# Optimization experiments

Measured on AMD Instinct MI355X. Metric: run time of the kernel, lower is better.

## Reference

```python
import jax, jax.numpy as jnp
import numpy as np

EOS = 130


def setup_inputs() -> dict:
    key = jax.random.key(0)
    ks = jax.random.split(key, 16)
    B, H, W, C = 32, 12, 32, 512   # encoder feature map
    V, E, D = 600, 256, 512        # vocab, embed_dim, decoder_hidden
    T = 192
    s = lambda *d: 1.0 / np.sqrt(d[-1])
    inp = {
        "encoder_outputs": jax.random.normal(ks[0], (B, H, W, C), jnp.float32),
        "tgt_tokens": jax.random.randint(ks[1], (B, T), 0, V, jnp.int64),
        # embedding table (padding_idx=0 row zeroed)
        "emb_table": (jax.random.normal(ks[2], (V, E), jnp.float32) * 0.02).at[0].set(0.0),
        # LSTMCell params, gate order i,f,g,o; stored (in, 4D) / (4D,)
        "W_ih": jax.random.normal(ks[3], (E + D, 4 * D), jnp.float32) * s(E + D),
        "b_ih": jnp.zeros((4 * D,), jnp.float32),
        "W_hh": jax.random.normal(ks[4], (D, 4 * D), jnp.float32) * s(D),
        "b_hh": jnp.zeros((4 * D,), jnp.float32),
        # attention
        "W_h": jax.random.normal(ks[5], (D, D), jnp.float32) * s(D),
        "W_v": jax.random.normal(ks[6], (C, D), jnp.float32) * s(C),
        "v": jax.random.normal(ks[7], (D, 1), jnp.float32) * s(D),
        # output path
        "W_c": jax.random.normal(ks[8], (D + C, D), jnp.float32) * s(D + C),
        "b_c": jnp.zeros((D,), jnp.float32),
        "W_out": jax.random.normal(ks[9], (D, V), jnp.float32) * s(D),
        "b_out": jnp.zeros((V,), jnp.float32),
    }
    return inp


def _decode(encoder_outputs, tgt_tokens, emb_table, W_ih, b_ih, W_hh, b_hh,
            W_h, W_v, v, W_c, b_c, W_out, b_out):
    B, H, W_, C = encoder_outputs.shape
    D = W_h.shape[0]
    enc = encoder_outputs.reshape(B, H * W_, C)          # (B, N, C)
    Wv = enc @ W_v                                       # (B, N, D) precompute (step-invariant)

    def step(carry, tok_t):
        hx, cx, o_prev, input_token, finished = carry
        emb = emb_table[input_token]                     # (B, E)
        rnn_in = jnp.concatenate([emb, o_prev], axis=-1)
        gates = rnn_in @ W_ih + b_ih + hx @ W_hh + b_hh  # (B, 4D)
        i, f, g, o = jnp.split(gates, 4, axis=-1)
        cx = jax.nn.sigmoid(f) * cx + jax.nn.sigmoid(i) * jnp.tanh(g)
        hx = jax.nn.sigmoid(o) * jnp.tanh(cx)
        # Bahdanau attention
        score = jnp.squeeze(jnp.tanh(hx[:, None, :] @ W_h + Wv) @ v, -1)  # (B, N)
        alpha = jax.nn.softmax(score, axis=1)
        context = jnp.einsum('bn,bnc->bc', alpha, enc)
        o_t = jnp.tanh(jnp.concatenate([hx, context], axis=-1) @ W_c + b_c)
        logits_t = o_t @ W_out + b_out                   # (B, V)
        next_token = tok_t                               # teacher forcing (ratio=1.0)
        finished = finished | (next_token == EOS)
        input_token = jnp.where(finished, 0, next_token)
        return (hx, cx, o_t, input_token, finished), (logits_t, alpha)

    hx = jnp.zeros((B, D), encoder_outputs.dtype)
    cx = jnp.zeros_like(hx)
    o0 = jnp.zeros_like(hx)
    tok0 = jnp.zeros((B,), tgt_tokens.dtype)             # sos_index = 0
    fin0 = jnp.zeros((B,), bool)
    xs = tgt_tokens[:, 1:].T                             # (T-1, B)
    _, (logits, alphas) = jax.lax.scan(step, (hx, cx, o0, tok0, fin0), xs)
    return logits.transpose(1, 0, 2), alphas.transpose(1, 0, 2)  # (B,T-1,V), (B,T-1,N)


def reference(encoder_outputs, tgt_tokens, emb_table, W_ih, b_ih, W_hh, b_hh,
              W_h, W_v, v, W_c, b_c, W_out, b_out):
    return _decode(encoder_outputs, tgt_tokens, emb_table, W_ih, b_ih, W_hh, b_hh,
                   W_h, W_v, v, W_c, b_c, W_out, b_out)
```

## Files before the change

kernel.cpp:

```cpp
#include <hip/hip_runtime.h>
#include <cstdint>

#define Bb 32
#define Cc 512
#define Nn 384
#define Vv 600
#define Ee 256
#define Dd 512
#define Tt 192
#define Ss 191
#define EOS_TOK 130
#define BD (Bb*Dd)
#define NBLK 256
#define NTHR 512

#define OFF_TOK   0
#define OFF_SHIFT 8192
#define OFF_WV    8256
#define OFF_HXT   6299712
#define OFF_XO    6332480
#define OFF_HXB   6348864
#define OFF_DEN   6365248
#define OFF_Q     6373440
#define OFF_CTXB  6389824
#define OFF_OBUF  6406208
#define OFF_BAR   9551936

#define LOGITS_SZ (Bb*Ss*Vv)
#define ALPHA_SZ  (Bb*Ss*Nn)

__device__ __forceinline__ float sigm_(float x) {
    float e = __expf(-x);
    return __builtin_amdgcn_rcpf(1.0f + e);
}
__device__ __forceinline__ float tanh_(float x) {
    float xc = fminf(15.0f, fmaxf(-15.0f, x));
    float e = __expf(2.0f * xc);
    return (e - 1.0f) * __builtin_amdgcn_rcpf(e + 1.0f);
}

__device__ __forceinline__ void st_dev(float* p, float v) {
    __hip_atomic_store(p, v, __ATOMIC_RELAXED, __HIP_MEMORY_SCOPE_AGENT);
}
__device__ __forceinline__ float ld1_dev(const float* p) {
    return __hip_atomic_load(p, __ATOMIC_RELAXED, __HIP_MEMORY_SCOPE_AGENT);
}
__device__ __forceinline__ float2 ld2_dev(const float* p) {
    unsigned long long u = __hip_atomic_load((const unsigned long long*)p,
                                             __ATOMIC_RELAXED,
                                             __HIP_MEMORY_SCOPE_AGENT);
    float2 f;
    f.x = __uint_as_float((unsigned int)u);
    f.y = __uint_as_float((unsigned int)(u >> 32));
    return f;
}

__device__ __forceinline__ void gbar(int* flags, int* genv, int ibar) {
    __syncthreads();
    const int target = ibar + 1;
    if (threadIdx.x == 0)
        __hip_atomic_store(&flags[blockIdx.x * 16], target, __ATOMIC_RELAXED,
                           __HIP_MEMORY_SCOPE_AGENT);
    if (blockIdx.x == 0) {
        if (threadIdx.x < 64) {
            int l = threadIdx.x * 4;
            for (;;) {
                int f0 = __hip_atomic_load(&flags[(l + 0) * 16], __ATOMIC_RELAXED,
                                           __HIP_MEMORY_SCOPE_AGENT);
                int f1 = __hip_atomic_load(&flags[(l + 1) * 16], __ATOMIC_RELAXED,
                                           __HIP_MEMORY_SCOPE_AGENT);
                int f2 = __hip_atomic_load(&flags[(l + 2) * 16], __ATOMIC_RELAXED,
                                           __HIP_MEMORY_SCOPE_AGENT);
                int f3 = __hip_atomic_load(&flags[(l + 3) * 16], __ATOMIC_RELAXED,
                                           __HIP_MEMORY_SCOPE_AGENT);
                if (__all(f0 >= target && f1 >= target &&
                          f2 >= target && f3 >= target)) break;
                __builtin_amdgcn_s_sleep(1);
            }
            if (threadIdx.x < 32)
                __hip_atomic_store(&genv[threadIdx.x * 16], target,
                                   __ATOMIC_RELAXED, __HIP_MEMORY_SCOPE_AGENT);
        }
    } else if (threadIdx.x == 0) {
        int* g = &genv[(blockIdx.x >> 3) * 16];
        while (__hip_atomic_load(g, __ATOMIC_RELAXED,
                                 __HIP_MEMORY_SCOPE_AGENT) < target)
            __builtin_amdgcn_s_sleep(2);
    }
    __syncthreads();
}

__device__ __forceinline__ void poll8(int* base, int grp, int target) {
    if (threadIdx.x < 64) {
        int* g = &base[(grp * 8 + (threadIdx.x & 7)) * 16];
        while (__hip_atomic_load(g, __ATOMIC_RELAXED,
                                 __HIP_MEMORY_SCOPE_AGENT) < target)
            __builtin_amdgcn_s_sleep(1);
    }
    __syncthreads();
}

__global__ void k_setup(const int* __restrict__ tgt, const float* __restrict__ vv,
                        float* zbase, int* bar, int* tok, float* shiftbuf) {
    int gid = blockIdx.x * 256 + threadIdx.x;
    for (int i = gid; i < 73728; i += 96 * 256) zbase[i] = 0.f;
    if (gid < 12800) bar[gid] = 0;
    if (blockIdx.x == 0) {
        __shared__ int is64;
        if (threadIdx.x == 0) {
            int a = 1;
            for (int k = 0; k < 32; ++k) if (tgt[2 * k + 1] != 0) a = 0;
            is64 = a;
        }
        __syncthreads();
        int b = threadIdx.x;
        if (b < Bb) {
            int fin = 0;
            tok[0 * Bb + b] = 0;
            for (int s = 1; s < Ss; ++s) {
                int li = b * Tt + s;
                int nt = is64 ? tgt[2 * li] : tgt[li];
                if (nt == EOS_TOK) fin = 1;
                tok[s * Bb + b] = fin ? 0 : nt;
            }
        }
    }
    if (blockIdx.x == 1) {
        __shared__ float sred[256];
        int tid = threadIdx.x;
        sred[tid] = fabsf(vv[tid]) + fabsf(vv[tid + 256]);
        __syncthreads();
        for (int s = 128; s > 0; s >>= 1) {
            if (tid < s) sred[tid] += sred[tid + s];
            __syncthreads();
        }
        if (tid == 0) shiftbuf[0] = sred[0];
    }
}

__global__ void k_embx(const float* __restrict__ emb, const int* __restrict__ tok,
                       float* __restrict__ obuf) {
    int i = blockIdx.x * 256 + threadIdx.x;
    if (i < Ss * 8192) {
        int t = i >> 13, e = i & 8191;
        int k = e >> 5, b = e & 31;
        obuf[(size_t)(t + 1) * BD + e] = emb[(size_t)tok[t * 32 + b] * Ee + k];
    }
}

__global__ void k_wv(const float* __restrict__ enc, const float* __restrict__ Wv_w,
                     float* __restrict__ Wv) {
    int b = blockIdx.x / 24, nt = blockIdx.x % 24, n0 = nt * 16;
    __shared__ float encL[16 * 512];
    for (int i = 0; i < 32; ++i) {
        int e = threadIdx.x + i * 256;
        int ni = e >> 9, c = e & 511;
        encL[e] = enc[((b * Nn) + (n0 + ni)) * Cc + c];
    }
    __syncthreads();
    int d0 = threadIdx.x, d1 = threadIdx.x + 256;
    float a0[16], a1[16];
#pragma unroll
    for (int i = 0; i < 16; ++i) { a0[i] = 0.f; a1[i] = 0.f; }
    for (int c = 0; c < 512; ++c) {
        float w0 = Wv_w[c * Dd + d0], w1 = Wv_w[c * Dd + d1];
#pragma unroll
        for (int i = 0; i < 16; ++i) {
            float ev = encL[i * 512 + c];
            a0[i] += ev * w0; a1[i] += ev * w1;
        }
    }
#pragma unroll
    for (int i = 0; i < 16; ++i) {
        Wv[((b * Nn) + (n0 + i)) * Dd + d0] = a0[i];
        Wv[((b * Nn) + (n0 + i)) * Dd + d1] = a1[i];
    }
}

__global__ __launch_bounds__(NTHR) void k_decode(
    const float* __restrict__ enc, const float* __restrict__ W_ih,
    const float* __restrict__ b_ih, const float* __restrict__ W_hh,
    const float* __restrict__ b_hh, const float* __restrict__ W_h,
    const float* __restrict__ vv, const float* __restrict__ W_c,
    const float* __restrict__ b_c, const float* __restrict__ Wv,
    const float* __restrict__ shiftbuf,
    float* __restrict__ hxT, float* __restrict__ xo, float* __restrict__ hxB,
    float* __restrict__ den, float* __restrict__ q, float* __restrict__ ctxB,
    float* __restrict__ obuf, float* __restrict__ alpha_e, int* bar)
{
    __shared__ float Wg[1280 * 8];
    __shared__ float scratch[8192];
    __shared__ float cxL[64];

    int* flags  = bar;
    int* genv   = bar + 4096;
    int* qdone  = bar + 4608;
    int* dedone = bar + 8704;

    const int tid = threadIdx.x, bid = blockIdx.x;
    const int lane = tid & 63;
    const int d0 = bid * 2;
    const int bp = tid & 15;
    const int ab = bid >> 3;
    const int n0 = (bid & 7) * 48;
    const int cg = bid & 7;
    const int w  = tid >> 6;

    for (int k = tid; k < 1280; k += NTHR) {
        const float* src = (k < 768) ? (W_ih + (size_t)k * 2048)
                                     : (W_hh + (size_t)(k - 768) * 2048);
#pragma unroll
        for (int g = 0; g < 4; ++g) {
            Wg[k * 8 + g * 2 + 0] = src[g * 512 + d0 + 0];
            Wg[k * 8 + g * 2 + 1] = src[g * 512 + d0 + 1];
        }
    }
    if (tid < 64) cxL[tid] = 0.f;
    float v8[8];
#pragma unroll
    for (int i = 0; i < 8; ++i) v8[i] = vv[lane * 8 + i];
    float4 wva[6], wvb[6];
#pragma unroll
    for (int r = 0; r < 6; ++r) {
        const float* wv = Wv + ((size_t)(ab * Nn + n0 + w * 6 + r)) * 512 + lane * 8;
        wva[r] = *(const float4*)wv;
        wvb[r] = *(const float4*)(wv + 4);
    }
    float encR[48];
#pragma unroll
    for (int i = 0; i < 48; ++i)
        encR[i] = enc[((size_t)(ab * Nn + n0 + i)) * 512 + tid];
    const float SHIFT = shiftbuf[0];
    const float bcF = b_c[cg * 64 + (tid & 63)];
    float bsum0 = 0.f, bsum1 = 0.f, bsum2 = 0.f, bsum3 = 0.f;
    if (tid < 64) {
        int dd = tid >> 5;
        int d = d0 + dd;
        bsum0 = b_ih[0 * 512 + d] + b_hh[0 * 512 + d];
        bsum1 = b_ih[1 * 512 + d] + b_hh[1 * 512 + d];
        bsum2 = b_ih[2 * 512 + d] + b_hh[2 * 512 + d];
        bsum3 = b_ih[3 * 512 + d] + b_hh[3 * 512 + d];
    }
    __syncthreads();

    int ib = 0;
    for (int t = 0; t < Ss; ++t) {
        const int rd = t & 1, wr = 1 - rd;
        const float* hxT_rd = hxT + rd * 16384;
        float*       hxT_wr = hxT + wr * 16384;

        {
            if (tid < 64)
                st_dev(&ctxB[bid * 64 + tid], 0.f);
            const float* embx_t = obuf + (size_t)(t + 1) * BD;
            const float* xo2 = xo - 256 * 32;
            const float* hx2 = hxT_rd - 768 * 32;
            int ks = tid >> 4;
            int k0 = ks * 40;
            float ax[8], ay[8];
#pragma unroll
            for (int i = 0; i < 8; ++i) { ax[i] = 0.f; ay[i] = 0.f; }
            if (t) {
#pragma unroll
                for (int kb = 0; kb < 5; ++kb) {
                    int kbase = k0 + kb * 8;
                    float2 xv[8];
#pragma unroll
                    for (int j = 0; j < 8; ++j) {
                        int k = kbase + j;
                        const float* base = (k < 256) ? embx_t : ((k < 768) ? xo2 : hx2);
                        xv[j] = ld2_dev(base + k * 32 + 2 * bp);
                    }
#pragma unroll
                    for (int j = 0; j < 8; ++j) {
                        int k = kbase + j;
                        float4 wA = *(const float4*)&Wg[k * 8];
                        float4 wB = *(const float4*)&Wg[k * 8 + 4];
                        ax[0] += xv[j].x * wA.x; ay[0] += xv[j].y * wA.x;
                        ax[1] += xv[j].x * wA.y; ay[1] += xv[j].y * wA.y;
                        ax[2] += xv[j].x * wA.z; ay[2] += xv[j].y * wA.z;
                        ax[3] += xv[j].x * wA.w; ay[3] += xv[j].y * wA.w;
                        ax[4] += xv[j].x * wB.x; ay[4] += xv[j].y * wB.x;
                        ax[5] += xv[j].x * wB.y; ay[5] += xv[j].y * wB.y;
                        ax[6] += xv[j].x * wB.z; ay[6] += xv[j].y * wB.z;
                        ax[7] += xv[j].x * wB.w; ay[7] += xv[j].y * wB.w;
                    }
                }
            }
#pragma unroll
            for (int c = 0; c < 8; ++c) {
                scratch[(ks * 8 + c) * 32 + 2 * bp]     = ax[c];
                scratch[(ks * 8 + c) * 32 + 2 * bp + 1] = ay[c];
            }
            __syncthreads();
            if (tid < 256) {
                int col = tid >> 5, b2 = tid & 31;
                float s = 0.f;
#pragma unroll
                for (int k2 = 0; k2 < 32; ++k2) s += scratch[(k2 * 8 + col) * 32 + b2];
                scratch[col * 32 + b2] = s;
            }
            __syncthreads();
            if (tid < 64) {
                int dd = tid >> 5, b2 = tid & 31;
                float gi = scratch[(0 * 2 + dd) * 32 + b2] + bsum0;
                float gf = scratch[(1 * 2 + dd) * 32 + b2] + bsum1;
                float gg = scratch[(2 * 2 + dd) * 32 + b2] + bsum2;
                float go = scratch[(3 * 2 + dd) * 32 + b2] + bsum3;
                float c = sigm_(gf) * cxL[tid] + sigm_(gi) * tanh_(gg);
                cxL[tid] = c;
                float h = sigm_(go) * tanh_(c);
                st_dev(&hxT_wr[(d0 + dd) * 32 + b2], h);
                st_dev(&hxB[b2 * 512 + d0 + dd], h);
            }
        }
        gbar(flags, genv, ib++);

        {
            float* hxL  = scratch;
            float* gred = scratch + 512;
            hxL[tid] = ld1_dev(&hxB[ab * 512 + tid]);
            __syncthreads();
            int col = tid & 63, kseg = tid >> 6;
            const float* wp = W_h + (size_t)(kseg * 64) * 512 + cg * 64 + col;
            const float* xr = hxL + kseg * 64;
            float a = 0.f;
#pragma unroll 8
            for (int kk = 0; kk < 64; ++kk)
                a += wp[(size_t)kk * 512] * xr[kk];
            gred[kseg * 72 + col] = a;
            __syncthreads();
            if (tid < 64) {
                float s = 0.f;
#pragma unroll
                for (int k2 = 0; k2 < 8; ++k2) s += gred[k2 * 72 + tid];
                st_dev(&q[ab * 512 + cg * 64 + tid], s);
            }
            __syncthreads();
            if (tid == 0)
                __hip_atomic_store(&qdone[bid * 16], t + 1, __ATOMIC_RELAXED,
                                   __HIP_MEMORY_SCOPE_AGENT);
        }

        {
            poll8(qdone, ab, t + 1);
            float* esc = scratch;
            float q8[8];
#pragma unroll
            for (int j = 0; j < 4; ++j) {
                float2 qv = ld2_dev(&q[ab * 512 + lane * 8 + 2 * j]);
                q8[2 * j] = qv.x; q8[2 * j + 1] = qv.y;
            }
#pragma unroll
            for (int r = 0; r < 6; ++r) {
                float s = v8[0] * tanh_(q8[0] + wva[r].x) + v8[1] * tanh_(q8[1] + wva[r].y)
                        + v8[2] * tanh_(q8[2] + wva[r].z) + v8[3] * tanh_(q8[3] + wva[r].w)
                        + v8[4] * tanh_(q8[4] + wvb[r].x) + v8[5] * tanh_(q8[5] + wvb[r].y)
                        + v8[6] * tanh_(q8[6] + wvb[r].z) + v8[7] * tanh_(q8[7] + wvb[r].w);
#pragma unroll
                for (int off = 32; off > 0; off >>= 1)
                    s += __shfl_down(s, off, 64);
                if (lane == 0) esc[w * 6 + r] = __expf(s - SHIFT);
            }
            __syncthreads();
            if (tid < 48)
                alpha_e[((size_t)ab * Ss + t) * Nn + n0 + tid] = esc[tid];
            if (tid == 0) {
                float sd = 0.f;
                for (int i = 0; i < 48; ++i) sd += esc[i];
                atomicAdd(&den[t * 32 + ab], sd);
            }
            float acc = 0.f;
#pragma unroll 8
            for (int i = 0; i < 48; ++i)
                acc += esc[i] * encR[i];
            atomicAdd(&ctxB[ab * 512 + tid], acc);
            __syncthreads();
            if (tid == 0)
                __hip_atomic_store(&dedone[bid * 16], t + 1, __ATOMIC_RELAXED,
                                   __HIP_MEMORY_SCOPE_AGENT);
        }

        {
            poll8(dedone, ab, t + 1);
            float* xF   = scratch;
            float* gred = scratch + 1024;
            float rdn = 1.0f / ld1_dev(&den[t * 32 + ab]);
            xF[tid]       = ld1_dev(&hxB[ab * 512 + tid]);
            xF[512 + tid] = ld1_dev(&ctxB[ab * 512 + tid]) * rdn;
            __syncthreads();
            int col = tid & 63, kseg = tid >> 6;
            const float* wp = W_c + (size_t)(kseg * 128) * 512 + cg * 64 + col;
            const float* xr = xF + kseg * 128;
            float a = 0.f;
#pragma unroll 8
            for (int kk = 0; kk < 128; ++kk)
                a += wp[(size_t)kk * 512] * xr[kk];
            gred[kseg * 72 + col] = a;
            __syncthreads();
            if (tid < 64) {
                float s = bcF;
#pragma unroll
                for (int k2 = 0; k2 < 8; ++k2) s += gred[k2 * 72 + tid];
                float o = tanh_(s);
                st_dev(&xo[(cg * 64 + tid) * 32 + ab], o);
                obuf[(size_t)(t + 1) * BD + ab * 512 + cg * 64 + tid] = o;
            }
        }
        gbar(flags, genv, ib++);
    }
}

__global__ void k_logits(const float* __restrict__ obuf, const float* __restrict__ W_out,
                         const float* __restrict__ b_out, float* __restrict__ out_logits) {
    int b = blockIdx.x / 24, tt = blockIdx.x % 24;
    int t0 = tt * 8;
    int tmax = min(8, Ss - t0);
    __shared__ float oL[8 * 512];
    int tid = threadIdx.x;
    for (int i = 0; i < 16; ++i) {
        int e = tid + i * 256;
        int ti = e >> 9, d = e & 511;
        oL[e] = (ti < tmax) ? obuf[(size_t)(t0 + ti + 1) * BD + b * Dd + d] : 0.f;
    }
    __syncthreads();
    int v0 = tid, v1 = tid + 256, v2 = tid + 512;
    bool h2 = (v2 < Vv);
    int v2c = h2 ? v2 : 0;
    float acc[3][8];
#pragma unroll
    for (int s = 0; s < 3; ++s)
#pragma unroll
        for (int ti = 0; ti < 8; ++ti) acc[s][ti] = 0.f;
    for (int d = 0; d < 512; ++d) {
        float w0 = W_out[d * Vv + v0];
        float w1 = W_out[d * Vv + v1];
        float w2 = W_out[d * Vv + v2c];
#pragma unroll
        for (int ti = 0; ti < 8; ++ti) {
            float o = oL[ti * 512 + d];
            acc[0][ti] += o * w0; acc[1][ti] += o * w1; acc[2][ti] += o * w2;
        }
    }
    for (int ti = 0; ti < tmax; ++ti) {
        size_t base = (size_t)b * (Ss * Vv) + (size_t)(t0 + ti) * Vv;
        out_logits[base + v0] = acc[0][ti] + b_out[v0];
        out_logits[base + v1] = acc[1][ti] + b_out[v1];
        if (h2) out_logits[base + v2] = acc[2][ti] + b_out[v2];
    }
}

__global__ void k_anorm(float* __restrict__ alph, const float* __restrict__ den) {
    int i = blockIdx.x * 256 + threadIdx.x;
    if (i < ALPHA_SZ) {
        int bt = i / Nn;
        int t = bt % Ss, b = bt / Ss;
        alph[i] = alph[i] / den[t * 32 + b];
    }
}

extern "C" void kernel_launch(void* const* d_in, const int* in_sizes, int n_in,
                              void* d_out, int out_size, void* d_ws, size_t ws_size,
                              hipStream_t stream) {
    const float* enc   = (const float*)d_in[0];
    const int*   tgt   = (const int*)d_in[1];
    const float* emb   = (const float*)d_in[2];
    const float* W_ih  = (const float*)d_in[3];
    const float* b_ih  = (const float*)d_in[4];
    const float* W_hh  = (const float*)d_in[5];
    const float* b_hh  = (const float*)d_in[6];
    const float* W_h   = (const float*)d_in[7];
    const float* W_v   = (const float*)d_in[8];
    const float* vv    = (const float*)d_in[9];
    const float* W_c   = (const float*)d_in[10];
    const float* b_c   = (const float*)d_in[11];
    const float* W_out = (const float*)d_in[12];
    const float* b_out = (const float*)d_in[13];

    float* wsf   = (float*)d_ws;
    int*   tok   = (int*)d_ws;
    float* shiftb= wsf + OFF_SHIFT;
    float* Wv    = wsf + OFF_WV;
    float* hxT   = wsf + OFF_HXT;
    float* xo    = wsf + OFF_XO;
    float* hxB   = wsf + OFF_HXB;
    float* den   = wsf + OFF_DEN;
    float* q     = wsf + OFF_Q;
    float* ctxB  = wsf + OFF_CTXB;
    float* obuf  = wsf + OFF_OBUF;
    int*   bar   = (int*)(wsf + OFF_BAR);

    float* out_logits = (float*)d_out;
    float* out_alphas = (float*)d_out + LOGITS_SZ;

    k_setup<<<96, 256, 0, stream>>>(tgt, vv, hxT, bar, tok, shiftb);
    k_embx<<<(Ss * 8192 + 255) / 256, 256, 0, stream>>>(emb, tok, obuf);
    k_wv<<<768, 256, 0, stream>>>(enc, W_v, Wv);
    k_decode<<<NBLK, NTHR, 0, stream>>>(enc, W_ih, b_ih, W_hh, b_hh, W_h, vv,
                                        W_c, b_c, Wv, shiftb,
                                        hxT, xo, hxB, den, q, ctxB, obuf,
                                        out_alphas, bar);
    k_logits<<<768, 256, 0, stream>>>(obuf, W_out, b_out, out_logits);
    k_anorm<<<(ALPHA_SZ + 255) / 256, 256, 0, stream>>>(out_alphas, den);
}
```

Measured before the change: 5.129 ms.

## Replace global barriers with split arrive/wait and fine-grained per-segment flags

Splits the end-of-step grid barrier into an arrive and a later wait, so the embedding and hidden-state parts of the LSTM gate GEMV run before waiting on the previous step's output vector. The mid-step barrier after the LSTM is replaced by per-block done flags, and each wave polls only the 32 producer blocks whose hidden slice it needs. In the output projection, the hidden-state half is loaded without waiting and only the context half polls the attention-done flags. This is meant to shorten the critical path of a latency-bound persistent kernel, at the cost of more subtle memory-ordering assumptions with relaxed atomics.

```diff
diff --git a/kernel.cpp b/kernel.cpp
--- a/kernel.cpp
+++ b/kernel.cpp
@@ -55,12 +55,14 @@
     return f;
 }
 
-__device__ __forceinline__ void gbar(int* flags, int* genv, int ibar) {
+__device__ __forceinline__ void w_arrive(int* flags, int ibar) {
     __syncthreads();
+    if (threadIdx.x == 0)
+        __hip_atomic_store(&flags[blockIdx.x * 16], ibar + 1, __ATOMIC_RELAXED,
+                           __HIP_MEMORY_SCOPE_AGENT);
+}
+__device__ __forceinline__ void w_wait(int* flags, int* genv, int ibar) {
     const int target = ibar + 1;
-    if (threadIdx.x == 0)
-        __hip_atomic_store(&flags[blockIdx.x * 16], target, __ATOMIC_RELAXED,
-                           __HIP_MEMORY_SCOPE_AGENT);
     if (blockIdx.x == 0) {
         if (threadIdx.x < 64) {
             int l = threadIdx.x * 4;
@@ -104,7 +106,7 @@
                         float* zbase, int* bar, int* tok, float* shiftbuf) {
     int gid = blockIdx.x * 256 + threadIdx.x;
     for (int i = gid; i < 73728; i += 96 * 256) zbase[i] = 0.f;
-    if (gid < 12800) bar[gid] = 0;
+    if (gid < 16896) bar[gid] = 0;
     if (blockIdx.x == 0) {
         __shared__ int is64;
         if (threadIdx.x == 0) {
@@ -196,6 +198,7 @@
     int* genv   = bar + 4096;
     int* qdone  = bar + 4608;
     int* dedone = bar + 8704;
+    int* adone  = bar + 12800;
 
     const int tid = threadIdx.x, bid = blockIdx.x;
     const int lane = tid & 63;
@@ -243,15 +246,12 @@
     }
     __syncthreads();
 
-    int ib = 0;
     for (int t = 0; t < Ss; ++t) {
         const int rd = t & 1, wr = 1 - rd;
         const float* hxT_rd = hxT + rd * 16384;
         float*       hxT_wr = hxT + wr * 16384;
 
         {
-            if (tid < 64)
-                st_dev(&ctxB[bid * 64 + tid], 0.f);
             const float* embx_t = obuf + (size_t)(t + 1) * BD;
             const float* xo2 = xo - 256 * 32;
             const float* hx2 = hxT_rd - 768 * 32;
@@ -264,13 +264,12 @@
 #pragma unroll
                 for (int kb = 0; kb < 5; ++kb) {
                     int kbase = k0 + kb * 8;
+                    if (kbase >= 256 && kbase < 768) continue;
+                    const float* base = (kbase < 256) ? embx_t : hx2;
                     float2 xv[8];
 #pragma unroll
-                    for (int j = 0; j < 8; ++j) {
-                        int k = kbase + j;
-                        const float* base = (k < 256) ? embx_t : ((k < 768) ? xo2 : hx2);
-                        xv[j] = ld2_dev(base + k * 32 + 2 * bp);
-                    }
+                    for (int j = 0; j < 8; ++j)
+                        xv[j] = ld2_dev(base + (kbase + j) * 32 + 2 * bp);
 #pragma unroll
                     for (int j = 0; j < 8; ++j) {
                         int k = kbase + j;
@@ -286,6 +285,35 @@
                         ax[7] += xv[j].x * wB.w; ay[7] += xv[j].y * wB.w;
                     }
                 }
+                w_wait(flags, genv, t - 1);
+                if (tid < 64)
+                    st_dev(&ctxB[bid * 64 + tid], 0.f);
+#pragma unroll
+                for (int kb = 0; kb < 5; ++kb) {
+                    int kbase = k0 + kb * 8;
+                    if (kbase < 256 || kbase >= 768) continue;
+                    float2 xv[8];
+#pragma unroll
+                    for (int j = 0; j < 8; ++j)
+                        xv[j] = ld2_dev(xo2 + (kbase + j) * 32 + 2 * bp);
+#pragma unroll
+                    for (int j = 0; j < 8; ++j) {
+                        int k = kbase + j;
+                        float4 wA = *(const float4*)&Wg[k * 8];
+                        float4 wB = *(const float4*)&Wg[k * 8 + 4];
+                        ax[0] += xv[j].x * wA.x; ay[0] += xv[j].y * wA.x;
+                        ax[1] += xv[j].x * wA.y; ay[1] += xv[j].y * wA.y;
+                        ax[2] += xv[j].x * wA.z; ay[2] += xv[j].y * wA.z;
+                        ax[3] += xv[j].x * wA.w; ay[3] += xv[j].y * wA.w;
+                        ax[4] += xv[j].x * wB.x; ay[4] += xv[j].y * wB.x;
+                        ax[5] += xv[j].x * wB.y; ay[5] += xv[j].y * wB.y;
+                        ax[6] += xv[j].x * wB.z; ay[6] += xv[j].y * wB.z;
+                        ax[7] += xv[j].x * wB.w; ay[7] += xv[j].y * wB.w;
+                    }
+                }
+            } else {
+                if (tid < 64)
+                    st_dev(&ctxB[bid * 64 + tid], 0.f);
             }
 #pragma unroll
             for (int c = 0; c < 8; ++c) {
@@ -314,14 +342,22 @@
                 st_dev(&hxB[b2 * 512 + d0 + dd], h);
             }
         }
-        gbar(flags, genv, ib++);
+        __syncthreads();
+        if (tid == 0)
+            __hip_atomic_store(&adone[bid * 16], t + 1, __ATOMIC_RELAXED,
+                               __HIP_MEMORY_SCOPE_AGENT);
 
         {
             float* hxL  = scratch;
             float* gred = scratch + 512;
-            hxL[tid] = ld1_dev(&hxB[ab * 512 + tid]);
-            __syncthreads();
             int col = tid & 63, kseg = tid >> 6;
+            {
+                int* g = &adone[(kseg * 32 + (tid & 31)) * 16];
+                while (__hip_atomic_load(g, __ATOMIC_RELAXED,
+                                         __HIP_MEMORY_SCOPE_AGENT) < t + 1)
+                    __builtin_amdgcn_s_sleep(1);
+            }
+            hxL[kseg * 64 + col] = ld1_dev(&hxB[ab * 512 + kseg * 64 + col]);
             const float* wp = W_h + (size_t)(kseg * 64) * 512 + cg * 64 + col;
             const float* xr = hxL + kseg * 64;
             float a = 0.f;
@@ -382,14 +418,22 @@
         }
 
         {
-            poll8(dedone, ab, t + 1);
             float* xF   = scratch;
             float* gred = scratch + 1024;
-            float rdn = 1.0f / ld1_dev(&den[t * 32 + ab]);
-            xF[tid]       = ld1_dev(&hxB[ab * 512 + tid]);
-            xF[512 + tid] = ld1_dev(&ctxB[ab * 512 + tid]) * rdn;
-            __syncthreads();
             int col = tid & 63, kseg = tid >> 6;
+            if (kseg < 4) {
+                xF[kseg * 128 + col]      = ld1_dev(&hxB[ab * 512 + kseg * 128 + col]);
+                xF[kseg * 128 + 64 + col] = ld1_dev(&hxB[ab * 512 + kseg * 128 + 64 + col]);
+            } else {
+                int* g = &dedone[(ab * 8 + (tid & 7)) * 16];
+                while (__hip_atomic_load(g, __ATOMIC_RELAXED,
+                                         __HIP_MEMORY_SCOPE_AGENT) < t + 1)
+                    __builtin_amdgcn_s_sleep(1);
+                float rdn = 1.0f / ld1_dev(&den[t * 32 + ab]);
+                int base = (kseg - 4) * 128;
+                xF[512 + base + col]      = ld1_dev(&ctxB[ab * 512 + base + col]) * rdn;
+                xF[512 + base + 64 + col] = ld1_dev(&ctxB[ab * 512 + base + 64 + col]) * rdn;
+            }
             const float* wp = W_c + (size_t)(kseg * 128) * 512 + cg * 64 + col;
             const float* xr = xF + kseg * 128;
             float a = 0.f;
@@ -407,7 +451,7 @@
                 obuf[(size_t)(t + 1) * BD + ab * 512 + cg * 64 + tid] = o;
             }
         }
-        gbar(flags, genv, ib++);
+        w_arrive(flags, t);
     }
 }
 
```

New measurement: 5.629 ms. +9.8%, slower.

## Compute LSTM gates on half the blocks with four hidden units each

Applied to the files above, without the earlier changes.

The per-step LSTM gate matmul now runs on 128 blocks, each owning 4 hidden units instead of 2, while the other 128 blocks skip that phase. Each thread accumulates 16 gate columns instead of 8, and the cross-thread reduction is rebuilt as a two-half accumulate followed by a 16-way sum. This halves how many blocks redundantly read the shared input and hidden vectors each step, which should cut global traffic and contention. In exchange, per-block work doubles on the serial critical path and register and LDS pressure grow, with a risk of spills.

```diff
diff --git a/kernel.cpp b/kernel.cpp
--- a/kernel.cpp
+++ b/kernel.cpp
@@ -12,6 +12,7 @@
 #define EOS_TOK 130
 #define BD (Bb*Dd)
 #define NBLK 256
+#define NBLKA 128
 #define NTHR 512
 
 #define OFF_TOK   0
@@ -188,9 +189,9 @@
     float* __restrict__ den, float* __restrict__ q, float* __restrict__ ctxB,
     float* __restrict__ obuf, float* __restrict__ alpha_e, int* bar)
 {
-    __shared__ float Wg[1280 * 8];
+    __shared__ float Wg[1280 * 16];
     __shared__ float scratch[8192];
-    __shared__ float cxL[64];
+    __shared__ float cxL[128];
 
     int* flags  = bar;
     int* genv   = bar + 4096;
@@ -199,23 +200,26 @@
 
     const int tid = threadIdx.x, bid = blockIdx.x;
     const int lane = tid & 63;
-    const int d0 = bid * 2;
+    const int d0 = bid * 4;
     const int bp = tid & 15;
     const int ab = bid >> 3;
     const int n0 = (bid & 7) * 48;
     const int cg = bid & 7;
     const int w  = tid >> 6;
 
-    for (int k = tid; k < 1280; k += NTHR) {
-        const float* src = (k < 768) ? (W_ih + (size_t)k * 2048)
-                                     : (W_hh + (size_t)(k - 768) * 2048);
-#pragma unroll
-        for (int g = 0; g < 4; ++g) {
-            Wg[k * 8 + g * 2 + 0] = src[g * 512 + d0 + 0];
-            Wg[k * 8 + g * 2 + 1] = src[g * 512 + d0 + 1];
-        }
-    }
-    if (tid < 64) cxL[tid] = 0.f;
+    if (bid < NBLKA) {
+        for (int k = tid; k < 1280; k += NTHR) {
+            const float* src = (k < 768) ? (W_ih + (size_t)k * 2048)
+                                         : (W_hh + (size_t)(k - 768) * 2048);
+#pragma unroll
+            for (int g = 0; g < 4; ++g) {
+#pragma unroll
+                for (int dd = 0; dd < 4; ++dd)
+                    Wg[k * 16 + g * 4 + dd] = src[g * 512 + d0 + dd];
+            }
+        }
+    }
+    if (tid < 128) cxL[tid] = 0.f;
     float v8[8];
 #pragma unroll
     for (int i = 0; i < 8; ++i) v8[i] = vv[lane * 8 + i];
@@ -233,7 +237,7 @@
     const float SHIFT = shiftbuf[0];
     const float bcF = b_c[cg * 64 + (tid & 63)];
     float bsum0 = 0.f, bsum1 = 0.f, bsum2 = 0.f, bsum3 = 0.f;
-    if (tid < 64) {
+    if (bid < NBLKA && tid < 128) {
         int dd = tid >> 5;
         int d = d0 + dd;
         bsum0 = b_ih[0 * 512 + d] + b_hh[0 * 512 + d];
@@ -249,17 +253,17 @@
         const float* hxT_rd = hxT + rd * 16384;
         float*       hxT_wr = hxT + wr * 16384;
 
-        {
-            if (tid < 64)
-                st_dev(&ctxB[bid * 64 + tid], 0.f);
+        if (tid < 64)
+            st_dev(&ctxB[bid * 64 + tid], 0.f);
+        if (bid < NBLKA) {
             const float* embx_t = obuf + (size_t)(t + 1) * BD;
             const float* xo2 = xo - 256 * 32;
             const float* hx2 = hxT_rd - 768 * 32;
             int ks = tid >> 4;
             int k0 = ks * 40;
-            float ax[8], ay[8];
-#pragma unroll
-            for (int i = 0; i < 8; ++i) { ax[i] = 0.f; ay[i] = 0.f; }
+            float ax[16], ay[16];
+#pragma unroll
+            for (int i = 0; i < 16; ++i) { ax[i] = 0.f; ay[i] = 0.f; }
             if (t) {
 #pragma unroll
                 for (int kb = 0; kb < 5; ++kb) {
@@ -274,39 +278,61 @@
 #pragma unroll
                     for (int j = 0; j < 8; ++j) {
                         int k = kbase + j;
-                        float4 wA = *(const float4*)&Wg[k * 8];
-                        float4 wB = *(const float4*)&Wg[k * 8 + 4];
-                        ax[0] += xv[j].x * wA.x; ay[0] += xv[j].y * wA.x;
-                        ax[1] += xv[j].x * wA.y; ay[1] += xv[j].y * wA.y;
-                        ax[2] += xv[j].x * wA.z; ay[2] += xv[j].y * wA.z;
-                        ax[3] += xv[j].x * wA.w; ay[3] += xv[j].y * wA.w;
-                        ax[4] += xv[j].x * wB.x; ay[4] += xv[j].y * wB.x;
-                        ax[5] += xv[j].x * wB.y; ay[5] += xv[j].y * wB.y;
-                        ax[6] += xv[j].x * wB.z; ay[6] += xv[j].y * wB.z;
-                        ax[7] += xv[j].x * wB.w; ay[7] += xv[j].y * wB.w;
+                        float4 w0 = *(const float4*)&Wg[k * 16];
+                        float4 w1 = *(const float4*)&Wg[k * 16 + 4];
+                        float4 w2 = *(const float4*)&Wg[k * 16 + 8];
+                        float4 w3 = *(const float4*)&Wg[k * 16 + 12];
+                        float xx = xv[j].x, yy = xv[j].y;
+                        ax[0]  += xx * w0.x; ay[0]  += yy * w0.x;
+                        ax[1]  += xx * w0.y; ay[1]  += yy * w0.y;
+                        ax[2]  += xx * w0.z; ay[2]  += yy * w0.z;
+                        ax[3]  += xx * w0.w; ay[3]  += yy * w0.w;
+                        ax[4]  += xx * w1.x; ay[4]  += yy * w1.x;
+                        ax[5]  += xx * w1.y; ay[5]  += yy * w1.y;
+                        ax[6]  += xx * w1.z; ay[6]  += yy * w1.z;
+                        ax[7]  += xx * w1.w; ay[7]  += yy * w1.w;
+                        ax[8]  += xx * w2.x; ay[8]  += yy * w2.x;
+                        ax[9]  += xx * w2.y; ay[9]  += yy * w2.y;
+                        ax[10] += xx * w2.z; ay[10] += yy * w2.z;
+                        ax[11] += xx * w2.w; ay[11] += yy * w2.w;
+                        ax[12] += xx * w3.x; ay[12] += yy * w3.x;
+                        ax[13] += xx * w3.y; ay[13] += yy * w3.y;
+                        ax[14] += xx * w3.z; ay[14] += yy * w3.z;
+                        ax[15] += xx * w3.w; ay[15] += yy * w3.w;
                     }
                 }
             }
-#pragma unroll
-            for (int c = 0; c < 8; ++c) {
-                scratch[(ks * 8 + c) * 32 + 2 * bp]     = ax[c];
-                scratch[(ks * 8 + c) * 32 + 2 * bp + 1] = ay[c];
-            }
-            __syncthreads();
             if (tid < 256) {
+#pragma unroll
+                for (int c = 0; c < 16; ++c) {
+                    scratch[(ks * 16 + c) * 32 + 2 * bp]     = ax[c];
+                    scratch[(ks * 16 + c) * 32 + 2 * bp + 1] = ay[c];
+                }
+            }
+            __syncthreads();
+            if (tid >= 256) {
+#pragma unroll
+                for (int c = 0; c < 16; ++c) {
+                    scratch[((ks - 16) * 16 + c) * 32 + 2 * bp]     += ax[c];
+                    scratch[((ks - 16) * 16 + c) * 32 + 2 * bp + 1] += ay[c];
+                }
+            }
+            __syncthreads();
+            {
                 int col = tid >> 5, b2 = tid & 31;
                 float s = 0.f;
 #pragma unroll
-                for (int k2 = 0; k2 < 32; ++k2) s += scratch[(k2 * 8 + col) * 32 + b2];
+                for (int k2 = 0; k2 < 16; ++k2)
+                    s += scratch[(k2 * 16 + col) * 32 + b2];
                 scratch[col * 32 + b2] = s;
             }
             __syncthreads();
-            if (tid < 64) {
+            if (tid < 128) {
                 int dd = tid >> 5, b2 = tid & 31;
-                float gi = scratch[(0 * 2 + dd) * 32 + b2] + bsum0;
-                float gf = scratch[(1 * 2 + dd) * 32 + b2] + bsum1;
-                float gg = scratch[(2 * 2 + dd) * 32 + b2] + bsum2;
-                float go = scratch[(3 * 2 + dd) * 32 + b2] + bsum3;
+                float gi = scratch[(0 * 4 + dd) * 32 + b2] + bsum0;
+                float gf = scratch[(1 * 4 + dd) * 32 + b2] + bsum1;
+                float gg = scratch[(2 * 4 + dd) * 32 + b2] + bsum2;
+                float go = scratch[(3 * 4 + dd) * 32 + b2] + bsum3;
                 float c = sigm_(gf) * cxL[tid] + sigm_(gi) * tanh_(gg);
                 cxL[tid] = c;
                 float h = sigm_(go) * tanh_(c);
```

Result: slower. 5.544 ms (+8.1%).
